# Kernel optimization log

Hardware: AMD Instinct MI355X
Metric: run time of the kernel (lower is better)

## Reference

```python
import jax, jax.numpy as jnp
import numpy as np

B, LC, LP, D, L = 16, 512, 2048, 256, 4


def setup_inputs() -> dict:
    key = jax.random.key(0)
    ks = jax.random.split(key, 24)
    s = 0.05
    return {
        'comp_feat': jax.random.normal(ks[0], (B, LC, D), jnp.float32),
        'comp_mask': jax.random.randint(ks[1], (B, LC), 0, 2, jnp.int32),
        'prot_feat': jax.random.normal(ks[2], (B, LP, D), jnp.float32),
        'prot_mask': jax.random.randint(ks[3], (B, LP), 0, 2, jnp.int32),
        'U': jax.random.normal(ks[4], (L, D, D), jnp.float32) * s,
        'W_p2c': jax.random.normal(ks[5], (L, D, D), jnp.float32) * s,
        'b_p2c': jnp.zeros((L, D), jnp.float32),
        'W_c2p': jax.random.normal(ks[6], (L, D, D), jnp.float32) * s,
        'b_c2p': jnp.zeros((L, D), jnp.float32),
        'W_hc': jax.random.normal(ks[7], (L, D, D), jnp.float32) * s,
        'b_hc': jnp.zeros((L, D), jnp.float32),
        'W_hp': jax.random.normal(ks[8], (L, D, D), jnp.float32) * s,
        'b_hp': jnp.zeros((L, D), jnp.float32),
        'W_ac': jax.random.normal(ks[9], (L, 2 * D), jnp.float32) * s,
        'b_ac': jnp.zeros((L,), jnp.float32),
        'W_ap': jax.random.normal(ks[10], (L, 2 * D), jnp.float32) * s,
        'b_ap': jnp.zeros((L,), jnp.float32),
        'W_cc': jax.random.normal(ks[11], (L * D, D), jnp.float32) * s,
        'b_cc': jnp.zeros((D,), jnp.float32),
        'W_cp': jax.random.normal(ks[12], (L * D, D), jnp.float32) * s,
        'b_cp': jnp.zeros((D,), jnp.float32),
    }


def _masked_softmax(scores, mask):
    # scores: [B, N], mask: [B, N] float 0/1
    e = jnp.exp(scores - jnp.max(scores, axis=-1, keepdims=True)) * mask
    return e / (jnp.sum(e, axis=-1, keepdims=True) + 1e-6)


def _forward(comp_feat, prot_feat, cm, pm, U, W_p2c, b_p2c, W_c2p, b_c2p,
             W_hc, b_hc, W_hp, b_hp, W_ac, b_ac, W_ap, b_ap,
             W_cc, b_cc, W_cp, b_cp):
    mask2d = cm[:, :, None] * pm[:, None, :]  # [B, LC, LP]
    comp_pools, prot_pools, comp_layers, prot_layers = [], [], [], []
    for i in range(L):
        # bilinear score + tanh + mask
        A = jnp.tanh(jnp.einsum('bcd,de,bpe->bcp', comp_feat, U[i], prot_feat)) * mask2d
        comp_cross = jnp.einsum('bcp,bpd->bcd', A, jnp.tanh(prot_feat @ W_p2c[i] + b_p2c[i]))
        prot_cross = jnp.einsum('bcp,bcd->bpd', A, jnp.tanh(comp_feat @ W_c2p[i] + b_c2p[i]))
        comp_comb = jnp.concatenate([jnp.tanh(comp_feat @ W_hc[i] + b_hc[i]), comp_cross], axis=2)
        prot_comb = jnp.concatenate([jnp.tanh(prot_feat @ W_hp[i] + b_hp[i]), prot_cross], axis=2)
        comp_layers.append(comp_comb)
        prot_layers.append(prot_comb)
        cw = _masked_softmax(jnp.einsum('bcd,d->bc', comp_comb, W_ac[i]) + b_ac[i], cm)
        pw = _masked_softmax(jnp.einsum('bpd,d->bp', prot_comb, W_ap[i]) + b_ap[i], pm)
        comp_pools.append(jnp.sum(comp_feat * cw[:, :, None], axis=1))
        prot_pools.append(jnp.sum(prot_feat * pw[:, :, None], axis=1))
    comp_layerwise = jnp.concatenate(comp_layers, axis=2)  # [B, LC, 2*D*L]
    prot_layerwise = jnp.concatenate(prot_layers, axis=2)  # [B, LP, 2*D*L]
    comp_final = jnp.concatenate(comp_pools, axis=1) @ W_cc + b_cc  # [B, D]
    prot_final = jnp.concatenate(prot_pools, axis=1) @ W_cp + b_cp  # [B, D]
    return comp_final, prot_final, comp_layerwise, prot_layerwise


def reference(comp_feat, comp_mask, prot_feat, prot_mask, U, W_p2c, b_p2c,
              W_c2p, b_c2p, W_hc, b_hc, W_hp, b_hp, W_ac, b_ac, W_ap, b_ap,
              W_cc, b_cc, W_cp, b_cp):
    cm = comp_mask.astype(jnp.float32)
    pm = prot_mask.astype(jnp.float32)
    return _forward(comp_feat, prot_feat, cm, pm, U, W_p2c, b_p2c, W_c2p, b_c2p,
                    W_hc, b_hc, W_hp, b_hp, W_ac, b_ac, W_ap, b_ap,
                    W_cc, b_cc, W_cp, b_cp)
```

## Files before the change

kernel.cpp:

```cpp
#include <hip/hip_runtime.h>

typedef unsigned short u16;
typedef __attribute__((ext_vector_type(8))) short short8;
typedef __attribute__((ext_vector_type(4))) float f32x4;

#define FLAG_BIAS   1
#define FLAG_TANH   2
#define FLAG_MASK   4
#define FLAG_BF16   8
#define FLAG_NSTORE 16
#define FLAG_TSTORE 32
#define FLAG_SPLITN 64
#define FLAG_SCORE  128

__device__ __forceinline__ float fast_tanh(float x) {
  return 1.f - 2.f / (__expf(2.f * x) + 1.f);
}

__device__ __forceinline__ u16 f2bf(float f) {
  unsigned u = __float_as_uint(f);
  return (u16)((u + 0x7fffu + ((u >> 16) & 1u)) >> 16);
}

__device__ __forceinline__ unsigned cvtpk(float lo, float hi) {
  unsigned r;
  asm("v_cvt_pk_bf16_f32 %0, %1, %2" : "=v"(r) : "v"(lo), "v"(hi));
  return r;
}

__device__ __forceinline__ void gload_lds16(const void* g, void* l) {
  __builtin_amdgcn_global_load_lds(
      (const __attribute__((address_space(1))) unsigned int*)g,
      (__attribute__((address_space(3))) unsigned int*)l, 16, 0, 0);
}

template <int BN, int TRX>
__global__ __launch_bounds__(256)
void gemm_nt(const u16* __restrict__ X, long long xbs, long long xls, int ldx,
             const u16* __restrict__ Y, long long ybs, long long yls, int ldy,
             void* __restrict__ Outv, long long obs, long long ols, int obase, int ldo,
             u16* __restrict__ Tout, long long tobs, long long tols, int tldo,
             int K, int gx, int gy, int flags,
             const float* __restrict__ bias,
             const int* __restrict__ rmask, int rms,
             const int* __restrict__ cmask, int cms,
             const float* __restrict__ sbase, float* __restrict__ sout,
             long long sls, int svoff, long long shs,
             const u16* __restrict__ Y2, const float* __restrict__ bias2,
             const float* __restrict__ sbase2, float* __restrict__ sout2,
             long long sls2, long long shs2, int msplit) {
  constexpr int NACC = BN / 32;
  constexpr int YB = BN * 32 * 2;
  constexpr int XB = TRX ? 8704 : 8192;
  constexpr int BUFB = XB + YB;
  constexpr int NBUF = TRX ? 2 : 3;
  constexpr int BW = BN + 4;
  constexpr int NSTB = 32 * BW * 4;
  constexpr int TSTB = (BN == 128 && !TRX) ? 64 * 132 * 4 : 0;
  constexpr int EPIB = (NSTB > TSTB) ? NSTB : TSTB;
  constexpr int SMEMB = (NBUF * BUFB > EPIB) ? NBUF * BUFB : EPIB;
  __shared__ __align__(16) char smem[SMEMB];
  const int t = threadIdx.x;
  const int lane = t & 63, wid = t >> 6;
  const int wr = (wid >> 1) * 64, wc = (wid & 1) * (BN / 2);
  const int lin = blockIdx.x;
  const int w = (lin & 7) * ((int)gridDim.x >> 3) + (lin >> 3);
  const int bx = w % gx;
  const int wy = w / gx;
  const int by = wy % gy;
  const int z = wy / gy;
  const int bz = z & 15, lz = z >> 4;
  const int rb = by * 128;
  const int cb = bx * BN;
  const bool dual = (msplit > 0) && (rb >= msplit);
  const u16* Yeff = dual ? Y2 : Y;
  const float* biasE = dual ? bias2 : bias;
  const float* sbaseE = dual ? sbase2 : sbase;
  float* soutE = dual ? sout2 : sout;
  const long long slsE = dual ? sls2 : sls;
  const long long shsE = dual ? shs2 : shs;
  const int gofs = dual ? msplit : 0;
  const u16* Xb = X + (size_t)bz * xbs + (size_t)lz * xls +
                  (TRX ? (size_t)rb : (size_t)rb * ldx);
  const u16* Yb = Yeff + (size_t)bz * ybs + (size_t)lz * yls + (size_t)cb * ldy;
  const int srow = t >> 2, scol = (t & 3) * 8;
  const int r16 = lane & 15, kh = (lane >> 4) * 8;

  f32x4 acc[4][NACC];
#pragma unroll
  for (int m = 0; m < 4; m++)
#pragma unroll
    for (int n = 0; n < NACC; n++) acc[m][n] = (f32x4){0.f, 0.f, 0.f, 0.f};

  auto stageY = [&](int buf, int kk) {
    char* dst = smem + buf * BUFB + XB + t * 16;
#pragma unroll
    for (int j = 0; j < YB / 4096; j++)
      gload_lds16(Yb + (size_t)(j * 64 + srow) * ldy + kk + scol, dst + j * 4096);
  };
  auto stageX = [&](int buf, int kk) {
    char* dst = smem + buf * BUFB + t * 16;
#pragma unroll
    for (int j = 0; j < 2; j++)
      gload_lds16(Xb + (size_t)(j * 64 + srow) * ldx + kk + scol, dst + j * 4096);
  };
  auto stage = [&](int buf, int kk) { stageX(buf, kk); stageY(buf, kk); };
  uint4 xa, xb2;
  const int tc0 = (t >> 4) * 2, tp8 = (t & 15) * 8;
  auto xload = [&](int kk) {
    xa  = *(const uint4*)&Xb[(size_t)(kk + tc0) * ldx + tp8];
    xb2 = *(const uint4*)&Xb[(size_t)(kk + tc0 + 1) * ldx + tp8];
  };
  auto xwrite = [&](int buf) {
    u16* xt = (u16*)(smem + buf * BUFB);
    const unsigned* a = (const unsigned*)&xa;
    const unsigned* b = (const unsigned*)&xb2;
#pragma unroll
    for (int w2 = 0; w2 < 4; w2++) {
      const unsigned lo = (a[w2] & 0xffffu) | (b[w2] << 16);
      const unsigned hi = (a[w2] >> 16) | (b[w2] & 0xffff0000u);
      *(unsigned*)&xt[(size_t)(tp8 + 2 * w2) * 34 + tc0] = lo;
      *(unsigned*)&xt[(size_t)(tp8 + 2 * w2 + 1) * 34 + tc0] = hi;
    }
  };

  const int nt = K >> 5;
  if constexpr (!TRX) {
    stage(0, 0);
    if (nt > 1) stage(1, 32);
    int cur = 0;
    for (int tt = 0; tt < nt; ++tt) {
      if (tt + 1 < nt) {
        if constexpr (BN == 128) asm volatile("s_waitcnt vmcnt(4)" ::: "memory");
        else                     asm volatile("s_waitcnt vmcnt(6)" ::: "memory");
      } else {
        asm volatile("s_waitcnt vmcnt(0)" ::: "memory");
      }
      __builtin_amdgcn_sched_barrier(0);
      __builtin_amdgcn_s_barrier();
      if (tt + 2 < nt) {
        int nxt = cur + 2; if (nxt >= 3) nxt -= 3;
        stage(nxt, (tt + 2) * 32);
      }
      const u16* lx = (const u16*)(smem + cur * BUFB);
      const u16* ly = (const u16*)(smem + cur * BUFB + XB);
      short8 av[4], bv[NACC];
#pragma unroll
      for (int m = 0; m < 4; m++) av[m] = *(const short8*)&lx[(wr + m * 16 + r16) * 32 + kh];
#pragma unroll
      for (int n = 0; n < NACC; n++) bv[n] = *(const short8*)&ly[(wc + n * 16 + r16) * 32 + kh];
#pragma unroll
      for (int m = 0; m < 4; m++)
#pragma unroll
        for (int n = 0; n < NACC; n++)
          acc[m][n] = __builtin_amdgcn_mfma_f32_16x16x32_bf16(av[m], bv[n], acc[m][n], 0, 0, 0);
      if (++cur >= 3) cur = 0;
    }
  } else {
    xload(0); stageY(0, 0); xwrite(0);
    __syncthreads();
    for (int tt = 0; tt < nt; ++tt) {
      const int cur = tt & 1;
      if (tt + 1 < nt) {
        xload((tt + 1) * 32);
        stageY(cur ^ 1, (tt + 1) * 32);
      }
      short8 av[4], bv[NACC];
      const u16* xt = (const u16*)(smem + cur * BUFB);
#pragma unroll
      for (int m = 0; m < 4; m++) {
        const u16* rp = &xt[(size_t)(wr + m * 16 + r16) * 34 + kh];
        unsigned* d = (unsigned*)&av[m];
        d[0] = *(const unsigned*)(rp);
        d[1] = *(const unsigned*)(rp + 2);
        d[2] = *(const unsigned*)(rp + 4);
        d[3] = *(const unsigned*)(rp + 6);
      }
      const u16* ly = (const u16*)(smem + cur * BUFB + XB);
#pragma unroll
      for (int n = 0; n < NACC; n++) bv[n] = *(const short8*)&ly[(wc + n * 16 + r16) * 32 + kh];
#pragma unroll
      for (int m = 0; m < 4; m++)
#pragma unroll
        for (int n = 0; n < NACC; n++)
          acc[m][n] = __builtin_amdgcn_mfma_f32_16x16x32_bf16(av[m], bv[n], acc[m][n], 0, 0, 0);
      if (tt + 1 < nt) xwrite(cur ^ 1);
      __syncthreads();
    }
  }

  if (flags & (FLAG_BIAS | FLAG_TANH | FLAG_MASK)) {
    float rmv[16];
    if (flags & FLAG_MASK) {
#pragma unroll
      for (int m = 0; m < 4; m++)
#pragma unroll
        for (int j = 0; j < 4; j++)
          rmv[m * 4 + j] =
              (float)rmask[(size_t)bz * rms + rb + wr + m * 16 + ((lane >> 4) << 2) + j];
    }
#pragma unroll
    for (int n = 0; n < NACC; n++) {
      const int c = cb + wc + n * 16 + r16;
      const float bcol = (flags & FLAG_BIAS) ? biasE[c] : 0.f;
      const float cmv = (flags & FLAG_MASK) ? (float)cmask[(size_t)bz * cms + c] : 1.f;
#pragma unroll
      for (int m = 0; m < 4; m++) {
#pragma unroll
        for (int j = 0; j < 4; j++) {
          float v = acc[m][n][j] + bcol;
          if (flags & FLAG_TANH) v = fast_tanh(v);
          if (flags & FLAG_MASK) v *= cmv * rmv[m * 4 + j];
          acc[m][n][j] = v;
        }
      }
    }
  }

  const size_t ocol = (flags & FLAG_SPLITN) ? (size_t)((cb >> 8) * 512 + (cb & 255))
                                            : (size_t)obase + (size_t)lz * ols + cb;
  const int lsc = (flags & FLAG_SPLITN) ? (cb >> 8) : lz;
  const int shalf = (cb >> 7) & 1;
  const float* svec = (flags & FLAG_SCORE)
      ? sbaseE + (size_t)lsc * 512 + svoff + ((flags & FLAG_SPLITN) ? (cb & 255) : cb)
      : nullptr;

  if (flags & FLAG_NSTORE) {
#pragma unroll
    for (int m = 0; m < 4; m++) {
      __syncthreads();
      float* bb = (float*)smem;
#pragma unroll
      for (int n = 0; n < NACC; n++)
#pragma unroll
        for (int j = 0; j < 4; j++)
          bb[(size_t)((wid >> 1) * 16 + ((lane >> 4) << 2) + j) * BW + wc + n * 16 + r16] =
              acc[m][n][j];
      __syncthreads();
      const int lr = t >> 3;
      const int c0 = (t & 7) * (BN / 8);
      const int g = rb + (lr >> 4) * 64 + m * 16 + (lr & 15);
      const float4* src = (const float4*)&bb[(size_t)lr * BW + c0];
      if (flags & FLAG_BF16) {
        u16* op = (u16*)Outv + (size_t)bz * obs + (size_t)g * ldo + ocol + c0;
#pragma unroll
        for (int q = 0; q < BN / 64; q++) {
          const float4 f0 = src[2 * q], f1 = src[2 * q + 1];
          uint4 u;
          u.x = cvtpk(f0.x, f0.y); u.y = cvtpk(f0.z, f0.w);
          u.z = cvtpk(f1.x, f1.y); u.w = cvtpk(f1.z, f1.w);
          ((uint4*)op)[q] = u;
        }
      } else {
        float* op = (float*)Outv + (size_t)bz * obs + (size_t)g * ldo + ocol + c0;
        float sp = 0.f;
#pragma unroll
        for (int q = 0; q < BN / 32; q++) {
          const float4 v = src[q];
          ((float4*)op)[q] = v;
          if (flags & FLAG_SCORE) {
            const float4 wv = *(const float4*)&svec[c0 + q * 4];
            sp += v.x * wv.x + v.y * wv.y + v.z * wv.z + v.w * wv.w;
          }
        }
        if (flags & FLAG_SCORE) {
          sp += __shfl_xor(sp, 1);
          sp += __shfl_xor(sp, 2);
          sp += __shfl_xor(sp, 4);
          if ((t & 7) == 0)
            soutE[(size_t)shalf * shsE + (size_t)lsc * slsE +
                  (size_t)bz * (gy * 128) + (g - gofs)] = sp;
        }
      }
    }
  }

  if constexpr (BN == 128 && !TRX) {
    if (flags & FLAG_TSTORE) {
#pragma unroll
      for (int np = 0; np < 2; np++) {
        __syncthreads();
        float* bb = (float*)smem;
#pragma unroll
        for (int q = 0; q < 2; q++) {
          const int n = np * 2 + q;
#pragma unroll
          for (int m = 0; m < 4; m++)
#pragma unroll
            for (int j = 0; j < 4; j++)
              bb[(size_t)((wid & 1) * 32 + q * 16 + r16) * 132 + wr + m * 16 + ((lane >> 4) << 2) + j] =
                  acc[m][n][j];
        }
        __syncthreads();
        const int lc = t >> 2, r0 = (t & 3) * 32;
        const int colg = cb + (lc >> 5) * 64 + (np * 2 + ((lc >> 4) & 1)) * 16 + (lc & 15);
        const float4* src = (const float4*)&bb[(size_t)lc * 132 + r0];
        u16* op = Tout + (size_t)lz * tols + (size_t)bz * tobs + (size_t)colg * tldo + rb + r0;
#pragma unroll
        for (int q = 0; q < 4; q++) {
          const float4 f0 = src[2 * q], f1 = src[2 * q + 1];
          uint4 u;
          u.x = cvtpk(f0.x, f0.y); u.y = cvtpk(f0.z, f0.w);
          u.z = cvtpk(f1.x, f1.y); u.w = cvtpk(f1.z, f1.w);
          ((uint4*)op)[q] = u;
        }
      }
    }
  }
}

__global__ void wtrans5(const float* __restrict__ iU, const float* __restrict__ iP2C,
                        const float* __restrict__ iC2P, const float* __restrict__ iHC,
                        const float* __restrict__ iHP,
                        u16* __restrict__ oU, u16* __restrict__ oP2C,
                        u16* __restrict__ oC2P, u16* __restrict__ oHC,
                        u16* __restrict__ oHP) {
  __shared__ float tl[32][33];
  const int which = blockIdx.z >> 2, l = blockIdx.z & 3;
  const float* in;
  u16* out;
  switch (which) {
    case 0: in = iU;   out = oU;   break;
    case 1: in = iP2C; out = oP2C; break;
    case 2: in = iC2P; out = oC2P; break;
    case 3: in = iHC;  out = oHC;  break;
    default: in = iHP; out = oHP;  break;
  }
  const size_t bo = (size_t)l * 256 * 256;
  const int c0 = blockIdx.x * 32, r0 = blockIdx.y * 32;
  for (int i = threadIdx.y; i < 32; i += 8)
    tl[i][threadIdx.x] = in[bo + (size_t)(r0 + i) * 256 + c0 + threadIdx.x];
  __syncthreads();
  for (int i = threadIdx.y; i < 32; i += 8)
    out[bo + (size_t)(c0 + i) * 256 + r0 + threadIdx.x] = f2bf(tl[threadIdx.x][i]);
}

__global__ void conv_both(const float* __restrict__ a, u16* __restrict__ oa, int n4a,
                          const float* __restrict__ b, u16* __restrict__ ob, int n4b) {
  int i = blockIdx.x * 256 + threadIdx.x;
  const float* in;
  u16* out;
  if (i < n4a) { in = a; out = oa; }
  else { i -= n4a; if (i >= n4b) return; in = b; out = ob; }
  const float4 v = ((const float4*)in)[i];
  ushort4 o;
  o.x = f2bf(v.x); o.y = f2bf(v.y); o.z = f2bf(v.z); o.w = f2bf(v.w);
  ((ushort4*)out)[i] = o;
}

__global__ __launch_bounds__(256)
void softmax_w(const float* __restrict__ sCt, const float* __restrict__ sCx,
               const float* __restrict__ sPt, const float* __restrict__ sPx,
               long long shsC, long long shsP,
               const int* __restrict__ cmask, const int* __restrict__ pmask,
               float* __restrict__ wC, float* __restrict__ wP) {
  const int l = blockIdx.x >> 4, b = blockIdx.x & 15, t = threadIdx.x;
  const int ntok = blockIdx.y ? 2048 : 512;
  const long long shs = blockIdx.y ? shsP : shsC;
  const float* st = blockIdx.y ? (sPt + l * 32768 + b * 2048) : (sCt + l * 8192 + b * 512);
  const float* sx = blockIdx.y ? (sPx + l * 32768 + b * 2048) : (sCx + l * 8192 + b * 512);
  const int* mk = blockIdx.y ? (pmask + b * 2048) : (cmask + b * 512);
  float* w = blockIdx.y ? (wP + l * 32768 + b * 2048) : (wC + l * 8192 + b * 512);
  __shared__ float red[256];
  __shared__ float e[2048];
  float m = -1e30f;
  for (int i = t; i < ntok; i += 256)
    m = fmaxf(m, st[i] + st[shs + i] + sx[i] + sx[shs + i]);
  red[t] = m;
  __syncthreads();
  for (int h = 128; h; h >>= 1) { if (t < h) red[t] = fmaxf(red[t], red[t + h]); __syncthreads(); }
  const float smax = red[0];
  __syncthreads();
  float sum = 0.f;
  for (int i = t; i < ntok; i += 256) {
    const float ev = __expf(st[i] + st[shs + i] + sx[i] + sx[shs + i] - smax) * (float)mk[i];
    e[i] = ev;
    sum += ev;
  }
  red[t] = sum;
  __syncthreads();
  for (int h = 128; h; h >>= 1) { if (t < h) red[t] += red[t + h]; __syncthreads(); }
  const float inv = 1.f / (red[0] + 1e-6f);
  for (int i = t; i < ntok; i += 256) w[i] = e[i] * inv;
}

__global__ __launch_bounds__(256)
void poolpart(const float* __restrict__ wC, const float* __restrict__ wP,
              const float* __restrict__ cfeat, const float* __restrict__ pfeat,
              float* __restrict__ partC, float* __restrict__ partP) {
  const int b = blockIdx.x, y = blockIdx.y, d = threadIdx.x;
  const float* feat;
  const float* wb;
  int ls, tok0;
  float* part;
  if (y < 4) {
    feat = cfeat + (size_t)b * 512 * 256;
    wb = wC + b * 512; ls = 8192; tok0 = y * 128;
    part = partC + ((size_t)b * 4 + y) * 1024;
  } else {
    const int ch = y - 4;
    feat = pfeat + (size_t)b * 2048 * 256;
    wb = wP + b * 2048; ls = 32768; tok0 = ch * 128;
    part = partP + ((size_t)b * 16 + ch) * 1024;
  }
  float a0 = 0.f, a1 = 0.f, a2 = 0.f, a3 = 0.f;
  for (int tok = tok0; tok < tok0 + 128; tok++) {
    const float f = feat[(size_t)tok * 256 + d];
    a0 += wb[tok] * f;
    a1 += wb[ls + tok] * f;
    a2 += wb[2 * ls + tok] * f;
    a3 += wb[3 * ls + tok] * f;
  }
  part[d] = a0; part[256 + d] = a1; part[512 + d] = a2; part[768 + d] = a3;
}

__global__ __launch_bounds__(1024)
void poolfinal(const float* __restrict__ partC, const float* __restrict__ partP,
               const float* __restrict__ W_cc, const float* __restrict__ b_cc,
               const float* __restrict__ W_cp, const float* __restrict__ b_cp,
               float* __restrict__ out_cf, float* __restrict__ out_pf) {
  const int b = blockIdx.x;
  const int tid = threadIdx.y * 256 + threadIdx.x;
  __shared__ float pool[1024];
  __shared__ float red[4][256];
  const float* part;
  const float* W;
  const float* bias;
  float* outp;
  int nch;
  if (blockIdx.y == 0) { part = partC + (size_t)b * 4 * 1024;  W = W_cc; bias = b_cc; outp = out_cf; nch = 4; }
  else                 { part = partP + (size_t)b * 16 * 1024; W = W_cp; bias = b_cp; outp = out_pf; nch = 16; }
  float s = 0.f;
  for (int ch = 0; ch < nch; ch++) s += part[(size_t)ch * 1024 + tid];
  pool[tid] = s;
  __syncthreads();
  const int n = threadIdx.x, q = threadIdx.y;
  float acc = 0.f;
  const float* w = W + (size_t)q * 256 * 256;
  const float* p = pool + q * 256;
  for (int k = 0; k < 256; k++) acc += p[k] * w[(size_t)k * 256 + n];
  red[q][n] = acc;
  __syncthreads();
  if (q == 0) outp[b * 256 + n] = red[0][n] + red[1][n] + red[2][n] + red[3][n] + bias[n];
}

static inline void launch_gemm(hipStream_t s, int BN, int TRX,
                               const u16* X, long long xbs, long long xls, int ldx,
                               const u16* Y, long long ybs, long long yls, int ldy,
                               void* Out, long long obs, long long ols, int obase, int ldo,
                               u16* Tout, long long tobs, long long tols, int tldo,
                               int M, int N, int K, int nz, int flags,
                               const float* bias, const int* rm, int rms,
                               const int* cm, int cms,
                               const float* sbase = nullptr, float* sout = nullptr,
                               long long sls = 0, int svoff = 0, long long shs = 0,
                               const u16* Y2 = nullptr, const float* bias2 = nullptr,
                               const float* sbase2 = nullptr, float* sout2 = nullptr,
                               long long sls2 = 0, long long shs2 = 0, int msplit = 0) {
  const int gx = N / BN, gy = M / 128;
  const int nb = gx * gy * nz;
  if (BN == 128 && !TRX)
    gemm_nt<128, 0><<<dim3(nb), dim3(256), 0, s>>>(X, xbs, xls, ldx, Y, ybs, yls, ldy,
                                                   Out, obs, ols, obase, ldo,
                                                   Tout, tobs, tols, tldo,
                                                   K, gx, gy, flags, bias, rm, rms, cm, cms,
                                                   sbase, sout, sls, svoff, shs,
                                                   Y2, bias2, sbase2, sout2, sls2, shs2, msplit);
  else if (!TRX)
    gemm_nt<256, 0><<<dim3(nb), dim3(256), 0, s>>>(X, xbs, xls, ldx, Y, ybs, yls, ldy,
                                                   Out, obs, ols, obase, ldo,
                                                   Tout, tobs, tols, tldo,
                                                   K, gx, gy, flags, bias, rm, rms, cm, cms,
                                                   sbase, sout, sls, svoff, shs,
                                                   Y2, bias2, sbase2, sout2, sls2, shs2, msplit);
  else
    gemm_nt<256, 1><<<dim3(nb), dim3(256), 0, s>>>(X, xbs, xls, ldx, Y, ybs, yls, ldy,
                                                   Out, obs, ols, obase, ldo,
                                                   Tout, tobs, tols, tldo,
                                                   K, gx, gy, flags, bias, rm, rms, cm, cms,
                                                   sbase, sout, sls, svoff, shs,
                                                   Y2, bias2, sbase2, sout2, sls2, shs2, msplit);
}

extern "C" void kernel_launch(void* const* d_in, const int* in_sizes, int n_in,
                              void* d_out, int out_size, void* d_ws, size_t ws_size,
                              hipStream_t stream) {
  (void)in_sizes; (void)n_in; (void)out_size; (void)ws_size;
  enum { Bc = 16, LCc = 512, LPc = 2048, Dc = 256, Lc = 4 };

  const float* comp_feat = (const float*)d_in[0];
  const int*   comp_mask = (const int*)d_in[1];
  const float* prot_feat = (const float*)d_in[2];
  const int*   prot_mask = (const int*)d_in[3];
  const float* U     = (const float*)d_in[4];
  const float* W_p2c = (const float*)d_in[5];
  const float* b_p2c = (const float*)d_in[6];
  const float* W_c2p = (const float*)d_in[7];
  const float* b_c2p = (const float*)d_in[8];
  const float* W_hc  = (const float*)d_in[9];
  const float* b_hc  = (const float*)d_in[10];
  const float* W_hp  = (const float*)d_in[11];
  const float* b_hp  = (const float*)d_in[12];
  const float* W_ac  = (const float*)d_in[13];
  const float* b_ac  = (const float*)d_in[14];
  const float* W_ap  = (const float*)d_in[15];
  const float* b_ap  = (const float*)d_in[16];
  const float* W_cc  = (const float*)d_in[17];
  const float* b_cc  = (const float*)d_in[18];
  const float* W_cp  = (const float*)d_in[19];
  const float* b_cp  = (const float*)d_in[20];

  float* out_cf = (float*)d_out;
  float* out_pf = out_cf + Bc * Dc;
  float* CLW = out_pf + Bc * Dc;
  float* PLW = CLW + (size_t)Bc * LCc * 2 * Dc * Lc;

  char* wsp = (char*)d_ws;
  size_t off = 0;
  auto carve = [&](size_t bytes) -> char* {
    char* p = wsp + off;
    off += (bytes + 255) & ~(size_t)255;
    return p;
  };
  u16* cfb   = (u16*)carve((size_t)Bc * LCc * Dc * 2);
  u16* pfb   = (u16*)carve((size_t)Bc * LPc * Dc * 2);
  u16* Utb   = (u16*)carve((size_t)Lc * Dc * Dc * 2);
  u16* Wp2ct = (u16*)carve((size_t)Lc * Dc * Dc * 2);
  u16* Wc2pt = (u16*)carve((size_t)Lc * Dc * Dc * 2);
  u16* Whct  = (u16*)carve((size_t)Lc * Dc * Dc * 2);
  u16* Whpt  = (u16*)carve((size_t)Lc * Dc * Dc * 2);
  u16* CU_all   = (u16*)carve((size_t)Bc * LCc * Lc * Dc * 2);
  u16* C2Pt_all = (u16*)carve((size_t)Bc * Lc * Dc * LCc * 2);
  u16* P2Ct_all = (u16*)carve((size_t)Bc * Lc * Dc * LPc * 2);
  u16* A_all  = (u16*)carve((size_t)Lc * Bc * LCc * LPc * 2);
  float* sCt = (float*)carve((size_t)2 * Lc * Bc * LCc * 4);
  float* sCx = (float*)carve((size_t)2 * Lc * Bc * LCc * 4);
  float* sPt = (float*)carve((size_t)2 * Lc * Bc * LPc * 4);
  float* sPx = (float*)carve((size_t)2 * Lc * Bc * LPc * 4);
  float* wCb = (float*)carve((size_t)Lc * Bc * LCc * 4);
  float* wPb = (float*)carve((size_t)Lc * Bc * LPc * 4);
  float* partC = (float*)carve((size_t)Bc * 4 * 1024 * 4);
  float* partP = (float*)carve((size_t)Bc * 16 * 1024 * 4);

  const long long shsC = (long long)Lc * Bc * LCc;
  const long long shsP = (long long)Lc * Bc * LPc;

  hipMemsetAsync(sPx + shsP, 0, (size_t)shsP * 4, stream);

  {
    const int n4a = Bc * LCc * Dc / 4, n4b = Bc * LPc * Dc / 4;
    conv_both<<<dim3((n4a + n4b + 255) / 256), dim3(256), 0, stream>>>(
        comp_feat, cfb, n4a, prot_feat, pfb, n4b);
  }
  wtrans5<<<dim3(8, 8, 20), dim3(32, 8), 0, stream>>>(U, W_p2c, W_c2p, W_hc, W_hp,
                                                      Utb, Wp2ct, Wc2pt, Whct, Whpt);

  const int LW = 2 * Dc * Lc;

  launch_gemm(stream, 128, 0, cfb, 0, 0, Dc, Utb, 0, 0, Dc,
              CU_all, 0, 0, 0, Lc * Dc, nullptr, 0, 0, 0,
              Bc * LCc, Lc * Dc, Dc, 1, FLAG_NSTORE | FLAG_BF16,
              nullptr, nullptr, 0, nullptr, 0);
  launch_gemm(stream, 128, 0, cfb, 0, 0, Dc, Whct, 0, 0, Dc,
              CLW, 0, 0, 0, LW, nullptr, 0, 0, 0,
              Bc * (LCc + LPc), Lc * Dc, Dc, 1,
              FLAG_NSTORE | FLAG_SPLITN | FLAG_BIAS | FLAG_TANH | FLAG_SCORE,
              b_hc, nullptr, 0, nullptr, 0, W_ac, sCt, (long long)Bc * LCc, 0, shsC,
              Whpt, b_hp, W_ap, sPt, (long long)Bc * LPc, shsP, Bc * LCc);
  launch_gemm(stream, 128, 0, cfb, (long long)LCc * Dc, 0, Dc, Wc2pt, 0, 0, Dc,
              nullptr, 0, 0, 0, 0,
              C2Pt_all, (long long)Lc * Dc * LCc, 0, LCc,
              LCc, Lc * Dc, Dc, Bc, FLAG_TSTORE | FLAG_BIAS | FLAG_TANH,
              b_c2p, nullptr, 0, nullptr, 0);
  launch_gemm(stream, 128, 0, pfb, (long long)LPc * Dc, 0, Dc, Wp2ct, 0, 0, Dc,
              nullptr, 0, 0, 0, 0,
              P2Ct_all, (long long)Lc * Dc * LPc, 0, LPc,
              LPc, Lc * Dc, Dc, Bc, FLAG_TSTORE | FLAG_BIAS | FLAG_TANH,
              b_p2c, nullptr, 0, nullptr, 0);

  launch_gemm(stream, 128, 0,
              CU_all, (long long)LCc * Lc * Dc, Dc, Lc * Dc,
              pfb, (long long)LPc * Dc, 0, Dc,
              A_all, (long long)LCc * LPc, (long long)Bc * LCc * LPc, 0, LPc,
              nullptr, 0, 0, 0,
              LCc, LPc, Dc, Bc * Lc,
              FLAG_NSTORE | FLAG_BF16 | FLAG_TANH | FLAG_MASK,
              nullptr, comp_mask, LCc, prot_mask, LPc);
  launch_gemm(stream, 128, 0,
              A_all, (long long)LCc * LPc, (long long)Bc * LCc * LPc, LPc,
              P2Ct_all, (long long)Lc * Dc * LPc, (long long)Dc * LPc, LPc,
              CLW, (long long)LCc * LW, 512, 256, LW, nullptr, 0, 0, 0,
              LCc, Dc, LPc, Bc * Lc, FLAG_NSTORE | FLAG_SCORE,
              nullptr, nullptr, 0, nullptr, 0, W_ac, sCx, (long long)Bc * LCc, 256, shsC);
  launch_gemm(stream, 256, 1,
              A_all, (long long)LCc * LPc, (long long)Bc * LCc * LPc, LPc,
              C2Pt_all, (long long)Lc * Dc * LCc, (long long)Dc * LCc, LCc,
              PLW, (long long)LPc * LW, 512, 256, LW, nullptr, 0, 0, 0,
              LPc, Dc, LCc, Bc * Lc, FLAG_NSTORE | FLAG_SCORE,
              nullptr, nullptr, 0, nullptr, 0, W_ap, sPx, (long long)Bc * LPc, 256, shsP);

  softmax_w<<<dim3(Lc * Bc, 2), dim3(256), 0, stream>>>(sCt, sCx, sPt, sPx, shsC, shsP,
                                                        comp_mask, prot_mask, wCb, wPb);
  poolpart<<<dim3(Bc, 20), dim3(256), 0, stream>>>(wCb, wPb, comp_feat, prot_feat, partC, partP);
  poolfinal<<<dim3(Bc, 2), dim3(256, 4), 0, stream>>>(partC, partP, W_cc, b_cc, W_cp, b_cp,
                                                      out_cf, out_pf);
}
```

Baseline: 534.0 us.

## Merge c2p/p2c projection GEMMs into one dual launch and fuse softmax into pooling

Adds an X2/Tout2 path to the dual-mode GEMM so the compound and protein tanh projections (C2P and P2C) run as a single launch, with rows split at msplit. The separate softmax kernel is folded into the pooling kernel, which recomputes max and sum per layer in each block and builds normalized weights in shared memory, so the wC/wP buffers are no longer written or read. This saves a launch and a round trip through global memory. In exchange, every pooling block repeats the full-length softmax reductions, which is redundant work, especially for the 2048-token protein side.

```diff
diff --git a/kernel.cpp b/kernel.cpp
--- a/kernel.cpp
+++ b/kernel.cpp
@@ -46,9 +46,11 @@
              const int* __restrict__ cmask, int cms,
              const float* __restrict__ sbase, float* __restrict__ sout,
              long long sls, int svoff, long long shs,
+             const u16* __restrict__ X2, long long xbs2,
              const u16* __restrict__ Y2, const float* __restrict__ bias2,
              const float* __restrict__ sbase2, float* __restrict__ sout2,
-             long long sls2, long long shs2, int msplit) {
+             long long sls2, long long shs2,
+             u16* __restrict__ Tout2, long long tobs2, int tldo2, int msplit) {
   constexpr int NACC = BN / 32;
   constexpr int YB = BN * 32 * 2;
   constexpr int XB = TRX ? 8704 : 8192;
@@ -73,15 +75,20 @@
   const int rb = by * 128;
   const int cb = bx * BN;
   const bool dual = (msplit > 0) && (rb >= msplit);
+  const u16* Xeff = dual ? X2 : X;
+  const long long xbsE = dual ? xbs2 : xbs;
   const u16* Yeff = dual ? Y2 : Y;
   const float* biasE = dual ? bias2 : bias;
   const float* sbaseE = dual ? sbase2 : sbase;
   float* soutE = dual ? sout2 : sout;
   const long long slsE = dual ? sls2 : sls;
   const long long shsE = dual ? shs2 : shs;
+  u16* ToutE = dual ? Tout2 : Tout;
+  const long long tobsE = dual ? tobs2 : tobs;
+  const int tldoE = dual ? tldo2 : tldo;
   const int gofs = dual ? msplit : 0;
-  const u16* Xb = X + (size_t)bz * xbs + (size_t)lz * xls +
-                  (TRX ? (size_t)rb : (size_t)rb * ldx);
+  const u16* Xb = Xeff + (size_t)bz * xbsE + (size_t)lz * xls +
+                  (TRX ? (size_t)(rb - gofs) : (size_t)(rb - gofs) * ldx);
   const u16* Yb = Yeff + (size_t)bz * ybs + (size_t)lz * yls + (size_t)cb * ldy;
   const int srow = t >> 2, scol = (t & 3) * 8;
   const int r16 = lane & 15, kh = (lane >> 4) * 8;
@@ -295,7 +302,8 @@
         const int lc = t >> 2, r0 = (t & 3) * 32;
         const int colg = cb + (lc >> 5) * 64 + (np * 2 + ((lc >> 4) & 1)) * 16 + (lc & 15);
         const float4* src = (const float4*)&bb[(size_t)lc * 132 + r0];
-        u16* op = Tout + (size_t)lz * tols + (size_t)bz * tobs + (size_t)colg * tldo + rb + r0;
+        u16* op = ToutE + (size_t)lz * tols + (size_t)bz * tobsE +
+                  (size_t)colg * tldoE + (rb - gofs) + r0;
 #pragma unroll
         for (int q = 0; q < 4; q++) {
           const float4 f0 = src[2 * q], f1 = src[2 * q + 1];
@@ -349,67 +357,70 @@
 }
 
 __global__ __launch_bounds__(256)
-void softmax_w(const float* __restrict__ sCt, const float* __restrict__ sCx,
-               const float* __restrict__ sPt, const float* __restrict__ sPx,
-               long long shsC, long long shsP,
-               const int* __restrict__ cmask, const int* __restrict__ pmask,
-               float* __restrict__ wC, float* __restrict__ wP) {
-  const int l = blockIdx.x >> 4, b = blockIdx.x & 15, t = threadIdx.x;
-  const int ntok = blockIdx.y ? 2048 : 512;
-  const long long shs = blockIdx.y ? shsP : shsC;
-  const float* st = blockIdx.y ? (sPt + l * 32768 + b * 2048) : (sCt + l * 8192 + b * 512);
-  const float* sx = blockIdx.y ? (sPx + l * 32768 + b * 2048) : (sCx + l * 8192 + b * 512);
-  const int* mk = blockIdx.y ? (pmask + b * 2048) : (cmask + b * 512);
-  float* w = blockIdx.y ? (wP + l * 32768 + b * 2048) : (wC + l * 8192 + b * 512);
-  __shared__ float red[256];
-  __shared__ float e[2048];
-  float m = -1e30f;
-  for (int i = t; i < ntok; i += 256)
-    m = fmaxf(m, st[i] + st[shs + i] + sx[i] + sx[shs + i]);
-  red[t] = m;
-  __syncthreads();
-  for (int h = 128; h; h >>= 1) { if (t < h) red[t] = fmaxf(red[t], red[t + h]); __syncthreads(); }
-  const float smax = red[0];
-  __syncthreads();
-  float sum = 0.f;
-  for (int i = t; i < ntok; i += 256) {
-    const float ev = __expf(st[i] + st[shs + i] + sx[i] + sx[shs + i] - smax) * (float)mk[i];
-    e[i] = ev;
-    sum += ev;
-  }
-  red[t] = sum;
-  __syncthreads();
-  for (int h = 128; h; h >>= 1) { if (t < h) red[t] += red[t + h]; __syncthreads(); }
-  const float inv = 1.f / (red[0] + 1e-6f);
-  for (int i = t; i < ntok; i += 256) w[i] = e[i] * inv;
-}
-
-__global__ __launch_bounds__(256)
-void poolpart(const float* __restrict__ wC, const float* __restrict__ wP,
-              const float* __restrict__ cfeat, const float* __restrict__ pfeat,
-              float* __restrict__ partC, float* __restrict__ partP) {
-  const int b = blockIdx.x, y = blockIdx.y, d = threadIdx.x;
+void poolsm(const float* __restrict__ sCt, const float* __restrict__ sCx,
+            const float* __restrict__ sPt, const float* __restrict__ sPx,
+            long long shsC, long long shsP,
+            const int* __restrict__ cmask, const int* __restrict__ pmask,
+            const float* __restrict__ cfeat, const float* __restrict__ pfeat,
+            float* __restrict__ partC, float* __restrict__ partP) {
+  const int b = blockIdx.x, y = blockIdx.y, t = threadIdx.x;
+  int ntok, ls, tok0;
+  long long shs;
+  const float *st, *sx;
+  const int* mk;
   const float* feat;
-  const float* wb;
-  int ls, tok0;
   float* part;
   if (y < 4) {
+    ntok = 512; ls = 8192; shs = shsC;
+    st = sCt + b * 512; sx = sCx + b * 512;
+    mk = cmask + b * 512;
     feat = cfeat + (size_t)b * 512 * 256;
-    wb = wC + b * 512; ls = 8192; tok0 = y * 128;
+    tok0 = y * 128;
     part = partC + ((size_t)b * 4 + y) * 1024;
   } else {
-    const int ch = y - 4;
+    ntok = 2048; ls = 32768; shs = shsP;
+    st = sPt + b * 2048; sx = sPx + b * 2048;
+    mk = pmask + b * 2048;
     feat = pfeat + (size_t)b * 2048 * 256;
-    wb = wP + b * 2048; ls = 32768; tok0 = ch * 128;
-    part = partP + ((size_t)b * 16 + ch) * 1024;
-  }
+    tok0 = (y - 4) * 128;
+    part = partP + ((size_t)b * 16 + (y - 4)) * 1024;
+  }
+  __shared__ float red[256];
+  __shared__ float minv[4][2];
+  __shared__ float e[4][128];
+  for (int l = 0; l < 4; l++) {
+    const float* s1 = st + (size_t)l * ls;
+    const float* s2 = sx + (size_t)l * ls;
+    float m = -1e30f;
+    for (int i = t; i < ntok; i += 256)
+      m = fmaxf(m, s1[i] + s1[shs + i] + s2[i] + s2[shs + i]);
+    red[t] = m;
+    __syncthreads();
+    for (int h = 128; h; h >>= 1) { if (t < h) red[t] = fmaxf(red[t], red[t + h]); __syncthreads(); }
+    const float smax = red[0];
+    __syncthreads();
+    float sum = 0.f;
+    for (int i = t; i < ntok; i += 256)
+      sum += __expf(s1[i] + s1[shs + i] + s2[i] + s2[shs + i] - smax) * (float)mk[i];
+    red[t] = sum;
+    __syncthreads();
+    for (int h = 128; h; h >>= 1) { if (t < h) red[t] += red[t + h]; __syncthreads(); }
+    if (t == 0) { minv[l][0] = smax; minv[l][1] = 1.f / (red[0] + 1e-6f); }
+    __syncthreads();
+  }
+  for (int i = t; i < 512; i += 256) {
+    const int l = i >> 7, j = i & 127, tk = tok0 + j;
+    const float* s1 = st + (size_t)l * ls;
+    const float* s2 = sx + (size_t)l * ls;
+    e[l][j] = __expf(s1[tk] + s1[shs + tk] + s2[tk] + s2[shs + tk] - minv[l][0]) *
+              (float)mk[tk] * minv[l][1];
+  }
+  __syncthreads();
+  const int d = t;
   float a0 = 0.f, a1 = 0.f, a2 = 0.f, a3 = 0.f;
-  for (int tok = tok0; tok < tok0 + 128; tok++) {
-    const float f = feat[(size_t)tok * 256 + d];
-    a0 += wb[tok] * f;
-    a1 += wb[ls + tok] * f;
-    a2 += wb[2 * ls + tok] * f;
-    a3 += wb[3 * ls + tok] * f;
+  for (int j = 0; j < 128; j++) {
+    const float f = feat[(size_t)(tok0 + j) * 256 + d];
+    a0 += e[0][j] * f; a1 += e[1][j] * f; a2 += e[2][j] * f; a3 += e[3][j] * f;
   }
   part[d] = a0; part[256 + d] = a1; part[512 + d] = a2; part[768 + d] = a3;
 }
@@ -454,9 +465,12 @@
                                const int* cm, int cms,
                                const float* sbase = nullptr, float* sout = nullptr,
                                long long sls = 0, int svoff = 0, long long shs = 0,
+                               const u16* X2 = nullptr, long long xbs2 = 0,
                                const u16* Y2 = nullptr, const float* bias2 = nullptr,
                                const float* sbase2 = nullptr, float* sout2 = nullptr,
-                               long long sls2 = 0, long long shs2 = 0, int msplit = 0) {
+                               long long sls2 = 0, long long shs2 = 0,
+                               u16* Tout2 = nullptr, long long tobs2 = 0, int tldo2 = 0,
+                               int msplit = 0) {
   const int gx = N / BN, gy = M / 128;
   const int nb = gx * gy * nz;
   if (BN == 128 && !TRX)
@@ -465,21 +479,24 @@
                                                    Tout, tobs, tols, tldo,
                                                    K, gx, gy, flags, bias, rm, rms, cm, cms,
                                                    sbase, sout, sls, svoff, shs,
-                                                   Y2, bias2, sbase2, sout2, sls2, shs2, msplit);
+                                                   X2, xbs2, Y2, bias2, sbase2, sout2,
+                                                   sls2, shs2, Tout2, tobs2, tldo2, msplit);
   else if (!TRX)
     gemm_nt<256, 0><<<dim3(nb), dim3(256), 0, s>>>(X, xbs, xls, ldx, Y, ybs, yls, ldy,
                                                    Out, obs, ols, obase, ldo,
                                                    Tout, tobs, tols, tldo,
                                                    K, gx, gy, flags, bias, rm, rms, cm, cms,
                                                    sbase, sout, sls, svoff, shs,
-                                                   Y2, bias2, sbase2, sout2, sls2, shs2, msplit);
+                                                   X2, xbs2, Y2, bias2, sbase2, sout2,
+                                                   sls2, shs2, Tout2, tobs2, tldo2, msplit);
   else
     gemm_nt<256, 1><<<dim3(nb), dim3(256), 0, s>>>(X, xbs, xls, ldx, Y, ybs, yls, ldy,
                                                    Out, obs, ols, obase, ldo,
                                                    Tout, tobs, tols, tldo,
                                                    K, gx, gy, flags, bias, rm, rms, cm, cms,
                                                    sbase, sout, sls, svoff, shs,
-                                                   Y2, bias2, sbase2, sout2, sls2, shs2, msplit);
+                                                   X2, xbs2, Y2, bias2, sbase2, sout2,
+                                                   sls2, shs2, Tout2, tobs2, tldo2, msplit);
 }
 
 extern "C" void kernel_launch(void* const* d_in, const int* in_sizes, int n_in,
@@ -537,8 +554,6 @@
   float* sCx = (float*)carve((size_t)2 * Lc * Bc * LCc * 4);
   float* sPt = (float*)carve((size_t)2 * Lc * Bc * LPc * 4);
   float* sPx = (float*)carve((size_t)2 * Lc * Bc * LPc * 4);
-  float* wCb = (float*)carve((size_t)Lc * Bc * LCc * 4);
-  float* wPb = (float*)carve((size_t)Lc * Bc * LPc * 4);
   float* partC = (float*)carve((size_t)Bc * 4 * 1024 * 4);
   float* partP = (float*)carve((size_t)Bc * 16 * 1024 * 4);
 
@@ -566,17 +581,16 @@
               Bc * (LCc + LPc), Lc * Dc, Dc, 1,
               FLAG_NSTORE | FLAG_SPLITN | FLAG_BIAS | FLAG_TANH | FLAG_SCORE,
               b_hc, nullptr, 0, nullptr, 0, W_ac, sCt, (long long)Bc * LCc, 0, shsC,
-              Whpt, b_hp, W_ap, sPt, (long long)Bc * LPc, shsP, Bc * LCc);
+              pfb, 0, Whpt, b_hp, W_ap, sPt, (long long)Bc * LPc, shsP,
+              nullptr, 0, 0, Bc * LCc);
   launch_gemm(stream, 128, 0, cfb, (long long)LCc * Dc, 0, Dc, Wc2pt, 0, 0, Dc,
               nullptr, 0, 0, 0, 0,
               C2Pt_all, (long long)Lc * Dc * LCc, 0, LCc,
-              LCc, Lc * Dc, Dc, Bc, FLAG_TSTORE | FLAG_BIAS | FLAG_TANH,
-              b_c2p, nullptr, 0, nullptr, 0);
-  launch_gemm(stream, 128, 0, pfb, (long long)LPc * Dc, 0, Dc, Wp2ct, 0, 0, Dc,
-              nullptr, 0, 0, 0, 0,
-              P2Ct_all, (long long)Lc * Dc * LPc, 0, LPc,
-              LPc, Lc * Dc, Dc, Bc, FLAG_TSTORE | FLAG_BIAS | FLAG_TANH,
-              b_p2c, nullptr, 0, nullptr, 0);
+              LCc + LPc, Lc * Dc, Dc, Bc, FLAG_TSTORE | FLAG_BIAS | FLAG_TANH,
+              b_c2p, nullptr, 0, nullptr, 0,
+              nullptr, nullptr, 0, 0, 0,
+              pfb, (long long)LPc * Dc, Wp2ct, b_p2c, nullptr, nullptr, 0, 0,
+              P2Ct_all, (long long)Lc * Dc * LPc, LPc, LCc);
 
   launch_gemm(stream, 128, 0,
               CU_all, (long long)LCc * Lc * Dc, Dc, Lc * Dc,
@@ -599,9 +613,9 @@
               LPc, Dc, LCc, Bc * Lc, FLAG_NSTORE | FLAG_SCORE,
               nullptr, nullptr, 0, nullptr, 0, W_ap, sPx, (long long)Bc * LPc, 256, shsP);
 
-  softmax_w<<<dim3(Lc * Bc, 2), dim3(256), 0, stream>>>(sCt, sCx, sPt, sPx, shsC, shsP,
-                                                        comp_mask, prot_mask, wCb, wPb);
-  poolpart<<<dim3(Bc, 20), dim3(256), 0, stream>>>(wCb, wPb, comp_feat, prot_feat, partC, partP);
+  poolsm<<<dim3(Bc, 20), dim3(256), 0, stream>>>(sCt, sCx, sPt, sPx, shsC, shsP,
+                                                 comp_mask, prot_mask,
+                                                 comp_feat, prot_feat, partC, partP);
   poolfinal<<<dim3(Bc, 2), dim3(256, 4), 0, stream>>>(partC, partP, W_cc, b_cc, W_cp, b_cp,
                                                       out_cf, out_pf);
 }
```

Measured after the change: 559.7 us. 1.05x slower.
